# Performance work log

Hardware: AMD Instinct MI355X
Metric: run time of the kernel (lower is better)

Reference implementation:

```python
import jax, jax.numpy as jnp
import numpy as np

P_MIN = 0.8        # minimum cumulative probability mass kept per row
THRESHOLD = 1e-10  # drop matches with probability below this
EPS = 1e-6         # distance clamp (matches dist.clamp(min=1e-6) in backward)

B, N, M, D = 4, 4096, 4096, 3


def setup_inputs() -> dict:
    key = jax.random.key(0)
    kx, ky = jax.random.split(key)
    x = jax.random.normal(kx, (B, N, D), dtype=jnp.float32)
    y = jax.random.normal(ky, (B, M, D), dtype=jnp.float32)
    return {"x": x, "y": y}


def _pairwise_dist(x, y):
    # ||x_i - y_j|| via Gram trick; avoids materializing [B,N,M,D] diff tensor.
    sq = (
        jnp.sum(x * x, axis=-1)[:, :, None]
        + jnp.sum(y * y, axis=-1)[:, None, :]
        - 2.0 * jnp.einsum("bnd,bmd->bnm", x, y)
    )
    return jnp.sqrt(jnp.maximum(sq, EPS * EPS))  # [B, N, M]


def _sparse_match_weights(d):
    # Row-wise soft matching probabilities over targets j.
    p = jax.nn.softmax(-d, axis=-1)  # [B, N, M]
    # Keep the most-probable entries per row until cumulative mass reaches P_MIN
    # (the dense, jit-friendly equivalent of the COO compaction in the kernel).
    order = jnp.argsort(-p, axis=-1)
    p_sorted = jnp.take_along_axis(p, order, axis=-1)
    csum = jnp.cumsum(p_sorted, axis=-1)
    keep_sorted = (csum - p_sorted) < P_MIN  # include entry that crosses P_MIN
    inv = jnp.argsort(order, axis=-1)
    keep = jnp.take_along_axis(keep_sorted, inv, axis=-1)
    return jnp.where(keep & (p > THRESHOLD), p, 0.0)  # sparse COO values, dense layout


def reference(x, y):
    d = _pairwise_dist(x, y)                     # [B, N, M]
    w = jax.lax.stop_gradient(_sparse_match_weights(d))  # weights are constants in bwd
    loss = jnp.sum(w * d)                        # scalar matching loss
    return loss
```

## Files before the change

### kernel.cpp

```cpp
#include <hip/hip_runtime.h>


#define MCOLS 4096
#define KPT   64
#define WPB   4
#define P_MIN 0.8f
#define CAP   512

template <int CTRL, int RM, int BM, bool BC>
__device__ __forceinline__ float dpp_mov0(float x) {
    return __int_as_float(__builtin_amdgcn_update_dpp(
        0, __float_as_int(x), CTRL, RM, BM, BC));
}
__device__ __forceinline__ float dppSum(float v) {
    v += dpp_mov0<0x111, 0xF, 0xF, true >(v);
    v += dpp_mov0<0x112, 0xF, 0xF, true >(v);
    v += dpp_mov0<0x114, 0xF, 0xF, true >(v);
    v += dpp_mov0<0x118, 0xF, 0xF, true >(v);
    v += dpp_mov0<0x142, 0xA, 0xF, false>(v);
    v += dpp_mov0<0x143, 0xC, 0xF, false>(v);
    return __int_as_float(__builtin_amdgcn_readlane(__float_as_int(v), 63));
}
__device__ __forceinline__ float dppMax(float v) {
    v = fmaxf(v, dpp_mov0<0x111, 0xF, 0xF, true >(v));
    v = fmaxf(v, dpp_mov0<0x112, 0xF, 0xF, true >(v));
    v = fmaxf(v, dpp_mov0<0x114, 0xF, 0xF, true >(v));
    v = fmaxf(v, dpp_mov0<0x118, 0xF, 0xF, true >(v));
    v = fmaxf(v, dpp_mov0<0x142, 0xA, 0xF, false>(v));
    v = fmaxf(v, dpp_mov0<0x143, 0xC, 0xF, false>(v));
    return __int_as_float(__builtin_amdgcn_readlane(__float_as_int(v), 63));
}

__global__ __launch_bounds__(WPB * 64) void apml_row_wave(
        const float* __restrict__ x, const float* __restrict__ y,
        float* __restrict__ out) {
    __shared__ __align__(16) float scomp[WPB * CAP];
    __shared__ float wacc[WPB];

    const int tid  = threadIdx.x;
    const int wid  = tid >> 6;
    const int lane = tid & 63;
    const int row  = blockIdx.x * WPB + wid;
    const int b    = row >> 12;

    const float x0 = x[row * 3 + 0];
    const float x1 = x[row * 3 + 1];
    const float x2 = x[row * 3 + 2];
    const float* yb = y + (size_t)b * MCOLS * 3;

    float p[KPT];
    float zl = 0.0f, pml = 0.0f, sal = 0.0f;
    #pragma unroll
    for (int k = 0; k < KPT; ++k) {
        const int j = k * 64 + lane;
        const float y0 = yb[j * 3 + 0];
        const float y1 = yb[j * 3 + 1];
        const float y2 = yb[j * 3 + 2];
        const float dx = x0 - y0, dy = x1 - y1, dz = x2 - y2;
        const float sq = fmaxf(dx * dx + dy * dy + dz * dz, 1e-12f);
        const float dd = sqrtf(sq);
        const float pk = __expf(-dd);
        p[k] = pk;
        zl  += pk;
        pml  = fmaxf(pml, pk);
        sal  = fmaf(pk, dd, sal);
    }
    const float Z       = dppSum(zl);
    const float pmax    = dppMax(pml);
    const float spd_all = dppSum(sal);
    const float target  = P_MIN * Z;
    const float pTop = __uint_as_float(__float_as_uint(pmax) + 1u);

    float ssl = 0.0f, ssh = pTop;
    {
        float eGl = 16.0f * dppSum(p[0] + p[1] + p[2] + p[3]);
        float eGh = 0.0f;
        for (int it = 0; it < 4; ++it) {
            float s;
            if (it & 1) {
                s = 0.5f * (ssl + ssh);
            } else {
                const float den = fmaxf(eGl - eGh, 1e-30f);
                s = ssl + (ssh - ssl) * ((eGl - target) / den);
            }
            if (!(s > ssl && s < ssh)) s = 0.5f * (ssl + ssh);
            if (!(s > ssl && s < ssh)) break;
            float m = 0.0f;
            #pragma unroll
            for (int q = 0; q < 4; ++q) m += (p[q] >= s) ? p[q] : 0.0f;
            m = 16.0f * dppSum(m);
            if (m >= target) { ssl = s; eGl = m; }
            else             { ssh = s; eGh = m; }
        }
    }
    const float wbw = ssh - ssl;
    const float seed_lo = fmaxf(ssl - wbw, 0.0f);
    const float seed_hi = fminf(ssh + wbw, pTop);

    float sl = 0.0f, sh = pTop;
    float Gl = Z,    Gh = 0.0f;
    int   Cl = MCOLS, Ch = 0;

    for (int it = 0; it < 12 && (Cl - Ch) > CAP; ++it) {
        float s;
        if      (it == 0) s = seed_lo;
        else if (it == 1) s = seed_hi;
        else if (it & 1)  s = 0.5f * (sl + sh);
        else {
            const float den = fmaxf(Gl - Gh, 1e-30f);
            s = sl + (sh - sl) * ((Gl - target) / den);
        }
        if (!(s > sl && s < sh)) s = 0.5f * (sl + sh);
        if (!(s > sl && s < sh)) break;

        float m = 0.0f;
        int   c = 0;
        #pragma unroll
        for (int k = 0; k < KPT; ++k) {
            const bool ge = (p[k] >= s);
            m += ge ? p[k] : 0.0f;
            c += (int)__popcll(__ballot(ge));
        }
        m = dppSum(m);
        if (m >= target) { sl = s; Gl = m; Cl = c; }
        else             { sh = s; Gh = m; Ch = c; }
    }

    int C = 0;
    float slo = 0.0f;
    #pragma unroll
    for (int k = 0; k < KPT; ++k) {
        const float pv = p[k];
        const bool below = (pv < sl);
        const float t = below ? pv : 1.0f;
        slo -= t * __logf(t);
        const bool band = !below && (pv < sh);
        const unsigned long long mk = __ballot(band);
        if (band) {
            const unsigned mlo = (unsigned)mk, mhi = (unsigned)(mk >> 32);
            const int within = __builtin_amdgcn_mbcnt_hi(
                                   mhi, __builtin_amdgcn_mbcnt_lo(mlo, 0));
            const int pos = C + within;
            if (pos < CAP) scomp[wid * CAP + pos] = pv;
        }
        C += (int)__popcll(mk);
    }
    const float S_lo = dppSum(slo);
    __builtin_amdgcn_s_waitcnt(0);
    float cp[8];
    bool  cv[8];
    #pragma unroll
    for (int q = 0; q < 8; ++q) {
        const int idx = q * 64 + lane;
        cv[q] = (idx < C) && (idx < CAP);
        cp[q] = cv[q] ? scomp[wid * CAP + idx] : 0.0f;
    }

    float pstar, mb = 0.0f;
    int   cnt = 1;
    bool  haveTie;

    if (C > CAP) {
        pstar = (sl > 0.0f) ? __uint_as_float(__float_as_uint(sl) - 1u) : 0.0f;
        haveTie = false;
    } else {
        float lo_s = sl, hi_s = sh, lo_G = Gl, hi_G = Gh;
        int   lo_C = Cl, hi_C = Ch;
        for (int it = 0; it < 10 && (lo_C - hi_C) > 2; ++it) {
            float s;
            if (it & 1) {
                s = 0.5f * (lo_s + hi_s);
            } else {
                const float den = fmaxf(lo_G - hi_G, 1e-30f);
                s = lo_s + (hi_s - lo_s) * ((lo_G - target) / den);
            }
            if (!(s > lo_s && s < hi_s)) s = 0.5f * (lo_s + hi_s);
            if (!(s > lo_s && s < hi_s)) break;

            float m = 0.0f;
            int   c = Ch;
            #pragma unroll
            for (int q = 0; q < 8; ++q) {
                const bool ge = cv[q] && (cp[q] >= s);
                m += ge ? cp[q] : 0.0f;
                c += (int)__popcll(__ballot(ge));
            }
            m = Gh + dppSum(m);
            if (m >= target) { lo_s = s; lo_G = m; lo_C = c; }
            else             { hi_s = s; hi_G = m; hi_C = c; }
        }

        float scur = hi_s, M = hi_G;
        bool ok = false;
        pstar = lo_s;
        for (int e = 0; e < 16; ++e) {
            float vl = 0.0f;
            #pragma unroll
            for (int q = 0; q < 8; ++q)
                vl = fmaxf(vl, (cv[q] && cp[q] < scur) ? cp[q] : 0.0f);
            const float v = dppMax(vl);
            if (!(v > 0.0f)) break;
            int cvn = 0;
            #pragma unroll
            for (int q = 0; q < 8; ++q)
                cvn += (int)__popcll(__ballot(cv[q] && (cp[q] == v)));
            const float Mn = M + v * (float)cvn;
            if (Mn >= target) { pstar = v; mb = M; cnt = cvn; ok = true; break; }
            M = Mn; scur = v;
        }
        haveTie = ok;
        if (!ok) {
            pstar = (lo_s > 0.0f) ? __uint_as_float(__float_as_uint(lo_s) - 1u)
                                  : 0.0f;
        }
    }

    float sble = 0.0f;
    #pragma unroll
    for (int q = 0; q < 8; ++q) {
        const float t = (cv[q] && (cp[q] <= pstar)) ? cp[q] : 1.0f;
        sble -= t * __logf(t);
    }
    const float S_band_le = dppSum(sble);

    const float spd = spd_all - S_lo - S_band_le;

    if (lane == 0) {
        float tie = 0.0f;
        if (haveTie) {
            const float R = (target - mb) / pstar;
            int q = (int)ceilf(R);
            if (q < 1) q = 1;
            if (q > cnt) q = cnt;
            tie = (float)q * pstar * (-__logf(pstar));
        }
        wacc[wid] = (spd + tie) / Z;
    }
    __syncthreads();
    if (tid == 0) {
        atomicAdd(out, wacc[0] + wacc[1] + wacc[2] + wacc[3]);
    }
}

extern "C" void kernel_launch(void* const* d_in, const int* in_sizes, int n_in,
                              void* d_out, int out_size, void* d_ws, size_t ws_size,
                              hipStream_t stream) {
    const float* x = (const float*)d_in[0];
    const float* y = (const float*)d_in[1];
    float* out = (float*)d_out;

    const int nrows = in_sizes[0] / 3;
    const int nblocks = nrows / WPB;

    hipMemsetAsync(out, 0, sizeof(float), stream);
    apml_row_wave<<<nblocks, WPB * 64, 0, stream>>>(x, y, out);
}
```

Measured before the change: 188.3 us.

## Evaluate two thresholds per pass in row threshold search and vectorize y loads

The coarse threshold search now tests two split points per pass over the 64 register-resident probabilities, computing mass via sum of min(p, s) identities, so fewer sequential passes and reductions are needed. The y points are loaded as float3, the distance uses fmas, and Gh is recomputed exactly from the final bracket. The band-entropy sum moves inside the non-overflow branch and the validity mask array is dropped. This adds per-pass arithmetic and an extra reduction, and it changes how the search converges, which may leave more candidates in the band.

```diff
diff --git a/kernel.cpp b/kernel.cpp
--- a/kernel.cpp
+++ b/kernel.cpp
@@ -46,18 +46,15 @@
     const float x0 = x[row * 3 + 0];
     const float x1 = x[row * 3 + 1];
     const float x2 = x[row * 3 + 2];
-    const float* yb = y + (size_t)b * MCOLS * 3;
+    const float3* yb3 = (const float3*)(y + (size_t)b * MCOLS * 3);
 
     float p[KPT];
     float zl = 0.0f, pml = 0.0f, sal = 0.0f;
     #pragma unroll
     for (int k = 0; k < KPT; ++k) {
-        const int j = k * 64 + lane;
-        const float y0 = yb[j * 3 + 0];
-        const float y1 = yb[j * 3 + 1];
-        const float y2 = yb[j * 3 + 2];
-        const float dx = x0 - y0, dy = x1 - y1, dz = x2 - y2;
-        const float sq = fmaxf(dx * dx + dy * dy + dz * dz, 1e-12f);
+        const float3 a = yb3[k * 64 + lane];
+        const float dx = x0 - a.x, dy = x1 - a.y, dz = x2 - a.z;
+        const float sq = fmaxf(fmaf(dz, dz, fmaf(dy, dy, dx * dx)), 1e-12f);
         const float dd = sqrtf(sq);
         const float pk = __expf(-dd);
         p[k] = pk;
@@ -93,48 +90,65 @@
             else             { ssh = s; eGh = m; }
         }
     }
-    const float wbw = ssh - ssl;
-    const float seed_lo = fmaxf(ssl - wbw, 0.0f);
-    const float seed_hi = fminf(ssh + wbw, pTop);
 
     float sl = 0.0f, sh = pTop;
     float Gl = Z,    Gh = 0.0f;
     int   Cl = MCOLS, Ch = 0;
 
-    for (int it = 0; it < 12 && (Cl - Ch) > CAP; ++it) {
-        float s;
-        if      (it == 0) s = seed_lo;
-        else if (it == 1) s = seed_hi;
-        else if (it & 1)  s = 0.5f * (sl + sh);
-        else {
+    for (int pass = 0; pass < 4 && (Cl - Ch) > CAP; ++pass) {
+        const float w = sh - sl;
+        float s1, s2;
+        if (pass == 0) {
+            s1 = (ssl > sl && ssl < sh) ? ssl : (sl + 0.333f * w);
+            s2 = (ssh > sl && ssh < sh) ? ssh : (sl + 0.667f * w);
+            if (s2 < s1) { const float t = s1; s1 = s2; s2 = t; }
+            if (s1 == s2) s2 = 0.5f * (s1 + sh);
+        } else {
+            const float sm_b = 0.5f * (sl + sh);
             const float den = fmaxf(Gl - Gh, 1e-30f);
-            s = sl + (sh - sl) * ((Gl - target) / den);
-        }
-        if (!(s > sl && s < sh)) s = 0.5f * (sl + sh);
-        if (!(s > sl && s < sh)) break;
-
-        float m = 0.0f;
-        int   c = 0;
+            float sm_i = sl + w * ((Gl - target) / den);
+            if (!(sm_i > sl && sm_i < sh)) sm_i = sm_b;
+            s1 = fminf(sm_b, sm_i); s2 = fmaxf(sm_b, sm_i);
+            if (s1 == s2) {
+                s1 = 0.5f * (sl + s1);
+                s2 = 0.5f * (s2 + sh);
+            }
+        }
+        if (!(s1 > sl && s2 < sh && s1 <= s2)) {
+            s1 = s2 = 0.5f * (sl + sh);
+            if (!(s1 > sl && s1 < sh)) break;
+        }
+
+        float mn1 = 0.0f, mn2 = 0.0f;
+        int   c1 = 0,     c2 = 0;
         #pragma unroll
         for (int k = 0; k < KPT; ++k) {
-            const bool ge = (p[k] >= s);
-            m += ge ? p[k] : 0.0f;
-            c += (int)__popcll(__ballot(ge));
-        }
-        m = dppSum(m);
-        if (m >= target) { sl = s; Gl = m; Cl = c; }
-        else             { sh = s; Gh = m; Ch = c; }
+            const float pk = p[k];
+            mn1 += fminf(pk, s1);
+            mn2 += fminf(pk, s2);
+            c1 += (int)__popcll(__ballot(pk >= s1));
+            c2 += (int)__popcll(__ballot(pk >= s2));
+        }
+        const float F1 = dppSum(mn1);
+        const float F2 = dppSum(mn2);
+        const float m1 = Z - F1 + s1 * (float)c1;
+        const float m2 = Z - F2 + s2 * (float)c2;
+        if (m2 >= target)      { sl = s2; Gl = m2; Cl = c2; }
+        else if (m1 >= target) { sl = s1; Gl = m1; Cl = c1;
+                                 sh = s2; Gh = m2; Ch = c2; }
+        else                   { sh = s1; Gh = m1; Ch = c1; }
     }
 
     int C = 0;
-    float slo = 0.0f;
+    float slo = 0.0f, ghr = 0.0f;
     #pragma unroll
     for (int k = 0; k < KPT; ++k) {
         const float pv = p[k];
         const bool below = (pv < sl);
         const float t = below ? pv : 1.0f;
         slo -= t * __logf(t);
-        const bool band = !below && (pv < sh);
+        ghr += (pv >= sh) ? pv : 0.0f;
+        const bool band = (!below) && (pv < sh);
         const unsigned long long mk = __ballot(band);
         if (band) {
             const unsigned mlo = (unsigned)mk, mhi = (unsigned)(mk >> 32);
@@ -146,17 +160,17 @@
         C += (int)__popcll(mk);
     }
     const float S_lo = dppSum(slo);
+    Gh = dppSum(ghr);
     __builtin_amdgcn_s_waitcnt(0);
     float cp[8];
-    bool  cv[8];
     #pragma unroll
     for (int q = 0; q < 8; ++q) {
         const int idx = q * 64 + lane;
-        cv[q] = (idx < C) && (idx < CAP);
-        cp[q] = cv[q] ? scomp[wid * CAP + idx] : 0.0f;
-    }
-
-    float pstar, mb = 0.0f;
+        const float v = scomp[wid * CAP + idx];
+        cp[q] = (idx < C) ? v : 0.0f;
+    }
+
+    float pstar, mb = 0.0f, S_band_le = 0.0f;
     int   cnt = 1;
     bool  haveTie;
 
@@ -181,7 +195,7 @@
             int   c = Ch;
             #pragma unroll
             for (int q = 0; q < 8; ++q) {
-                const bool ge = cv[q] && (cp[q] >= s);
+                const bool ge = (cp[q] >= s);
                 m += ge ? cp[q] : 0.0f;
                 c += (int)__popcll(__ballot(ge));
             }
@@ -197,13 +211,13 @@
             float vl = 0.0f;
             #pragma unroll
             for (int q = 0; q < 8; ++q)
-                vl = fmaxf(vl, (cv[q] && cp[q] < scur) ? cp[q] : 0.0f);
+                vl = fmaxf(vl, (cp[q] < scur) ? cp[q] : 0.0f);
             const float v = dppMax(vl);
             if (!(v > 0.0f)) break;
             int cvn = 0;
             #pragma unroll
             for (int q = 0; q < 8; ++q)
-                cvn += (int)__popcll(__ballot(cv[q] && (cp[q] == v)));
+                cvn += (int)__popcll(__ballot(cp[q] == v));
             const float Mn = M + v * (float)cvn;
             if (Mn >= target) { pstar = v; mb = M; cnt = cvn; ok = true; break; }
             M = Mn; scur = v;
@@ -213,15 +227,15 @@
             pstar = (lo_s > 0.0f) ? __uint_as_float(__float_as_uint(lo_s) - 1u)
                                   : 0.0f;
         }
-    }
-
-    float sble = 0.0f;
-    #pragma unroll
-    for (int q = 0; q < 8; ++q) {
-        const float t = (cv[q] && (cp[q] <= pstar)) ? cp[q] : 1.0f;
-        sble -= t * __logf(t);
-    }
-    const float S_band_le = dppSum(sble);
+
+        float sble = 0.0f;
+        #pragma unroll
+        for (int q = 0; q < 8; ++q) {
+            const float t = (cp[q] > 0.0f && cp[q] <= pstar) ? cp[q] : 1.0f;
+            sble -= t * __logf(t);
+        }
+        S_band_le = dppSum(sble);
+    }
 
     const float spd = spd_all - S_lo - S_band_le;
 
```

Result: slower. 206.4 us (+9.6%).

## Store per-row probabilities as packed fp16 to halve register footprint

Applied to the files above, without the earlier changes.

Per-lane probabilities are now kept as packed half-precision pairs, clamped to a floor, instead of 64 fp32 registers. The register file pressure drops, which allows the launch bound to request 5 waves per SIMD, and the compaction buffer is halved. The seed bracket widening is removed and the band sums are recomputed during compaction. The trade-off is reduced precision in the threshold search and entropy terms, since the values used are rounded and clamped rather than exact fp32 probabilities, which can change which entries are kept.

```diff
diff --git a/kernel.cpp b/kernel.cpp
--- a/kernel.cpp
+++ b/kernel.cpp
@@ -2,10 +2,13 @@
 
 
 #define MCOLS 4096
-#define KPT   64
+#define KPT2  32
 #define WPB   4
 #define P_MIN 0.8f
-#define CAP   512
+#define CAP   256
+#define PCLAMP 6.2e-5f
+
+typedef __attribute__((ext_vector_type(2))) __fp16 f16x2;
 
 template <int CTRL, int RM, int BM, bool BC>
 __device__ __forceinline__ float dpp_mov0(float x) {
@@ -31,7 +34,7 @@
     return __int_as_float(__builtin_amdgcn_readlane(__float_as_int(v), 63));
 }
 
-__global__ __launch_bounds__(WPB * 64) void apml_row_wave(
+__global__ __launch_bounds__(WPB * 64, 5) void apml_row_wave(
         const float* __restrict__ x, const float* __restrict__ y,
         float* __restrict__ out) {
     __shared__ __align__(16) float scomp[WPB * CAP];
@@ -48,32 +51,37 @@
     const float x2 = x[row * 3 + 2];
     const float* yb = y + (size_t)b * MCOLS * 3;
 
-    float p[KPT];
-    float zl = 0.0f, pml = 0.0f, sal = 0.0f;
+    f16x2 ph[KPT2];
+    float zl = 0.0f, sal = 0.0f;
     #pragma unroll
-    for (int k = 0; k < KPT; ++k) {
-        const int j = k * 64 + lane;
-        const float y0 = yb[j * 3 + 0];
-        const float y1 = yb[j * 3 + 1];
-        const float y2 = yb[j * 3 + 2];
-        const float dx = x0 - y0, dy = x1 - y1, dz = x2 - y2;
-        const float sq = fmaxf(dx * dx + dy * dy + dz * dz, 1e-12f);
-        const float dd = sqrtf(sq);
-        const float pk = __expf(-dd);
-        p[k] = pk;
-        zl  += pk;
-        pml  = fmaxf(pml, pk);
-        sal  = fmaf(pk, dd, sal);
+    for (int k = 0; k < KPT2; ++k) {
+        const int j0 = (2 * k) * 64 + lane;
+        const int j1 = j0 + 64;
+        float ya = yb[j0 * 3 + 0], yc = yb[j0 * 3 + 1], ye = yb[j0 * 3 + 2];
+        float dx = x0 - ya, dy = x1 - yc, dz = x2 - ye;
+        const float sq0 = fmaxf(dx * dx + dy * dy + dz * dz, 1e-12f);
+        const float d0 = sqrtf(sq0);
+        const float p0 = __expf(-d0);
+        ya = yb[j1 * 3 + 0]; yc = yb[j1 * 3 + 1]; ye = yb[j1 * 3 + 2];
+        dx = x0 - ya; dy = x1 - yc; dz = x2 - ye;
+        const float sq1 = fmaxf(dx * dx + dy * dy + dz * dz, 1e-12f);
+        const float d1 = sqrtf(sq1);
+        const float p1 = __expf(-d1);
+        zl += p0 + p1;
+        sal = fmaf(p0, d0, sal);
+        sal = fmaf(p1, d1, sal);
+        ph[k] = __builtin_amdgcn_cvt_pkrtz(fmaxf(p0, PCLAMP),
+                                           fmaxf(p1, PCLAMP));
     }
     const float Z       = dppSum(zl);
-    const float pmax    = dppMax(pml);
     const float spd_all = dppSum(sal);
     const float target  = P_MIN * Z;
-    const float pTop = __uint_as_float(__float_as_uint(pmax) + 1u);
-
-    float ssl = 0.0f, ssh = pTop;
+
+    float ssl = 0.0f, ssh = 1.0f;
     {
-        float eGl = 16.0f * dppSum(p[0] + p[1] + p[2] + p[3]);
+        const float w0 = (float)ph[0].x, w1 = (float)ph[0].y;
+        const float w2 = (float)ph[1].x, w3 = (float)ph[1].y;
+        float eGl = 16.0f * dppSum(w0 + w1 + w2 + w3);
         float eGh = 0.0f;
         for (int it = 0; it < 4; ++it) {
             float s;
@@ -86,25 +94,24 @@
             if (!(s > ssl && s < ssh)) s = 0.5f * (ssl + ssh);
             if (!(s > ssl && s < ssh)) break;
             float m = 0.0f;
-            #pragma unroll
-            for (int q = 0; q < 4; ++q) m += (p[q] >= s) ? p[q] : 0.0f;
+            m += (w0 >= s) ? w0 : 0.0f;
+            m += (w1 >= s) ? w1 : 0.0f;
+            m += (w2 >= s) ? w2 : 0.0f;
+            m += (w3 >= s) ? w3 : 0.0f;
             m = 16.0f * dppSum(m);
             if (m >= target) { ssl = s; eGl = m; }
             else             { ssh = s; eGh = m; }
         }
     }
-    const float wbw = ssh - ssl;
-    const float seed_lo = fmaxf(ssl - wbw, 0.0f);
-    const float seed_hi = fminf(ssh + wbw, pTop);
-
-    float sl = 0.0f, sh = pTop;
+
+    float sl = 0.0f, sh = 1.0f;
     float Gl = Z,    Gh = 0.0f;
     int   Cl = MCOLS, Ch = 0;
 
     for (int it = 0; it < 12 && (Cl - Ch) > CAP; ++it) {
         float s;
-        if      (it == 0) s = seed_lo;
-        else if (it == 1) s = seed_hi;
+        if      (it == 0) s = ssl;
+        else if (it == 1) s = ssh;
         else if (it & 1)  s = 0.5f * (sl + sh);
         else {
             const float den = fmaxf(Gl - Gh, 1e-30f);
@@ -116,10 +123,14 @@
         float m = 0.0f;
         int   c = 0;
         #pragma unroll
-        for (int k = 0; k < KPT; ++k) {
-            const bool ge = (p[k] >= s);
-            m += ge ? p[k] : 0.0f;
-            c += (int)__popcll(__ballot(ge));
+        for (int k = 0; k < KPT2; ++k) {
+            const float f0 = (float)ph[k].x;
+            const float f1 = (float)ph[k].y;
+            const bool g0 = (f0 >= s), g1 = (f1 >= s);
+            m += g0 ? f0 : 0.0f;
+            m += g1 ? f1 : 0.0f;
+            c += (int)__popcll(__ballot(g0));
+            c += (int)__popcll(__ballot(g1));
         }
         m = dppSum(m);
         if (m >= target) { sl = s; Gl = m; Cl = c; }
@@ -127,36 +138,40 @@
     }
 
     int C = 0;
-    float slo = 0.0f;
+    float slo = 0.0f, ghr = 0.0f;
     #pragma unroll
-    for (int k = 0; k < KPT; ++k) {
-        const float pv = p[k];
-        const bool below = (pv < sl);
-        const float t = below ? pv : 1.0f;
-        slo -= t * __logf(t);
-        const bool band = !below && (pv < sh);
-        const unsigned long long mk = __ballot(band);
-        if (band) {
-            const unsigned mlo = (unsigned)mk, mhi = (unsigned)(mk >> 32);
-            const int within = __builtin_amdgcn_mbcnt_hi(
-                                   mhi, __builtin_amdgcn_mbcnt_lo(mlo, 0));
-            const int pos = C + within;
-            if (pos < CAP) scomp[wid * CAP + pos] = pv;
-        }
-        C += (int)__popcll(mk);
+    for (int k = 0; k < KPT2; ++k) {
+        #pragma unroll
+        for (int h = 0; h < 2; ++h) {
+            const float pv = h ? (float)ph[k].y : (float)ph[k].x;
+            const bool below = (pv < sl);
+            const float t = below ? pv : 1.0f;
+            slo -= t * __logf(t);
+            ghr += (pv >= sh) ? pv : 0.0f;
+            const bool band = (!below) && (pv < sh);
+            const unsigned long long mk = __ballot(band);
+            if (band) {
+                const unsigned mlo = (unsigned)mk, mhi = (unsigned)(mk >> 32);
+                const int within = __builtin_amdgcn_mbcnt_hi(
+                                       mhi, __builtin_amdgcn_mbcnt_lo(mlo, 0));
+                const int pos = C + within;
+                if (pos < CAP) scomp[wid * CAP + pos] = pv;
+            }
+            C += (int)__popcll(mk);
+        }
     }
     const float S_lo = dppSum(slo);
+    Gh = dppSum(ghr);
     __builtin_amdgcn_s_waitcnt(0);
-    float cp[8];
-    bool  cv[8];
+    float cp[4];
     #pragma unroll
-    for (int q = 0; q < 8; ++q) {
+    for (int q = 0; q < 4; ++q) {
         const int idx = q * 64 + lane;
-        cv[q] = (idx < C) && (idx < CAP);
-        cp[q] = cv[q] ? scomp[wid * CAP + idx] : 0.0f;
-    }
-
-    float pstar, mb = 0.0f;
+        const float v = scomp[wid * CAP + idx];
+        cp[q] = (idx < C) ? v : 0.0f;
+    }
+
+    float pstar, mb = 0.0f, S_band_le = 0.0f;
     int   cnt = 1;
     bool  haveTie;
 
@@ -180,8 +195,8 @@
             float m = 0.0f;
             int   c = Ch;
             #pragma unroll
-            for (int q = 0; q < 8; ++q) {
-                const bool ge = cv[q] && (cp[q] >= s);
+            for (int q = 0; q < 4; ++q) {
+                const bool ge = (cp[q] >= s);
                 m += ge ? cp[q] : 0.0f;
                 c += (int)__popcll(__ballot(ge));
             }
@@ -196,14 +211,14 @@
         for (int e = 0; e < 16; ++e) {
             float vl = 0.0f;
             #pragma unroll
-            for (int q = 0; q < 8; ++q)
-                vl = fmaxf(vl, (cv[q] && cp[q] < scur) ? cp[q] : 0.0f);
+            for (int q = 0; q < 4; ++q)
+                vl = fmaxf(vl, (cp[q] < scur) ? cp[q] : 0.0f);
             const float v = dppMax(vl);
             if (!(v > 0.0f)) break;
             int cvn = 0;
             #pragma unroll
-            for (int q = 0; q < 8; ++q)
-                cvn += (int)__popcll(__ballot(cv[q] && (cp[q] == v)));
+            for (int q = 0; q < 4; ++q)
+                cvn += (int)__popcll(__ballot(cp[q] == v));
             const float Mn = M + v * (float)cvn;
             if (Mn >= target) { pstar = v; mb = M; cnt = cvn; ok = true; break; }
             M = Mn; scur = v;
@@ -213,15 +228,15 @@
             pstar = (lo_s > 0.0f) ? __uint_as_float(__float_as_uint(lo_s) - 1u)
                                   : 0.0f;
         }
-    }
-
-    float sble = 0.0f;
-    #pragma unroll
-    for (int q = 0; q < 8; ++q) {
-        const float t = (cv[q] && (cp[q] <= pstar)) ? cp[q] : 1.0f;
-        sble -= t * __logf(t);
-    }
-    const float S_band_le = dppSum(sble);
+
+        float sble = 0.0f;
+        #pragma unroll
+        for (int q = 0; q < 4; ++q) {
+            const float t = (cp[q] > 0.0f && cp[q] <= pstar) ? cp[q] : 1.0f;
+            sble -= t * __logf(t);
+        }
+        S_band_le = dppSum(sble);
+    }
 
     const float spd = spd_all - S_lo - S_band_le;
 
@@ -252,6 +267,6 @@
     const int nrows = in_sizes[0] / 3;
     const int nblocks = nrows / WPB;
 
-    hipMemsetAsync(out, 0, sizeof(float), stream);
+    (void)hipMemsetAsync(out, 0, sizeof(float), stream);
     apml_row_wave<<<nblocks, WPB * 64, 0, stream>>>(x, y, out);
 }
```

Result: slower. 197.3 us (+4.8%).
